# Performance work log

Measured on AMD Instinct MI355X. Metric: run time of the kernel, lower is better.

The kernel has to match this reference:

```python
import jax, jax.numpy as jnp
import numpy as np

B = 4096   # batch_size from init_kwargs
D = 128    # embedding dim
TEMP = 0.25


def _l2_normalize(x, eps=1e-12):
    # matches F.normalize(dim=1): x / max(||x||, eps)
    n = jnp.linalg.norm(x, axis=1, keepdims=True)
    return x / jnp.maximum(n, eps)


def setup_inputs() -> dict:
    key = jax.random.key(0)
    k1, k2 = jax.random.split(key)
    return {
        "emb_i": jax.random.normal(k1, (B, D), dtype=jnp.float32),
        "emb_j": jax.random.normal(k2, (B, D), dtype=jnp.float32),
    }


def reference(emb_i, emb_j):
    b = emb_i.shape[0]
    z_i = _l2_normalize(emb_i)
    z_j = _l2_normalize(emb_j)
    reps = jnp.concatenate([z_i, z_j], axis=0)            # [2B, D]
    # cosine similarity of normalized vectors == dot product
    sim = reps @ reps.T                                    # [2B, 2B]
    sim_ij = jnp.diagonal(sim, offset=b)                   # [B]
    sim_ji = jnp.diagonal(sim, offset=-b)                  # [B]
    positives = jnp.concatenate([sim_ij, sim_ji], axis=0)  # [2B]
    # negatives_mask as overwritten in __init__: ones only on the two
    # off-diagonal cross-view blocks.
    mask = (
        jnp.zeros((2 * b, 2 * b), dtype=sim.dtype)
        .at[:b, b:].set(1.0)
        .at[b:, :b].set(1.0)
    )
    exp_sim = jnp.exp(sim / TEMP)                          # [2B, 2B]
    denom = jnp.sum(mask * exp_sim, axis=1)                # [2B]
    loss_partial = -jnp.log(jnp.exp(positives / TEMP) / denom)
    loss = jnp.sum(loss_partial) / (2 * b)
    return loss
```

## Files before the change

kernel.cpp:

```cpp
#include <hip/hip_runtime.h>
#include <hip/hip_bf16.h>

#define BATCH 4096
#define DIM   128
#define EXP_SCALE 5.770780163555854f

typedef __bf16 bf16_t;
typedef __bf16 bf16x8 __attribute__((ext_vector_type(8)));
typedef float  f32x4  __attribute__((ext_vector_type(4)));

__global__ __launch_bounds__(256) void normalize_kernel(
    const float* __restrict__ emb_i, const float* __restrict__ emb_j,
    bf16_t* __restrict__ zi, bf16_t* __restrict__ zj, float* __restrict__ pos)
{
    int wave = threadIdx.x >> 6;
    int lane = threadIdx.x & 63;
    int k = blockIdx.x * 4 + wave;

    const float2* ei = (const float2*)(emb_i + (size_t)k * DIM);
    const float2* ej = (const float2*)(emb_j + (size_t)k * DIM);
    float2 a = ei[lane];
    float2 b = ej[lane];

    float sii = a.x * a.x + a.y * a.y;
    float sjj = b.x * b.x + b.y * b.y;
    float sij = a.x * b.x + a.y * b.y;
#pragma unroll
    for (int m = 1; m < 64; m <<= 1) {
        sii += __shfl_xor(sii, m);
        sjj += __shfl_xor(sjj, m);
        sij += __shfl_xor(sij, m);
    }
    float inv_i = 1.0f / fmaxf(sqrtf(sii), 1e-12f);
    float inv_j = 1.0f / fmaxf(sqrtf(sjj), 1e-12f);

    struct bf16_2 { bf16_t x, y; };
    bf16_2 pi, pj;
    pi.x = (bf16_t)(a.x * inv_i);  pi.y = (bf16_t)(a.y * inv_i);
    pj.x = (bf16_t)(b.x * inv_j);  pj.y = (bf16_t)(b.y * inv_j);
    ((bf16_2*)(zi + (size_t)k * DIM))[lane] = pi;
    ((bf16_2*)(zj + (size_t)k * DIM))[lane] = pj;

    if (lane == 0) pos[k] = sij * inv_i * inv_j;
}

__global__ __launch_bounds__(256) void gemm_exp_kernel(
    const bf16_t* __restrict__ zi, const bf16_t* __restrict__ zj,
    float* __restrict__ rowDenom, float* __restrict__ colDenom)
{
    __shared__ __align__(16) bf16_t zi_s[128][136];
    __shared__ __align__(16) bf16_t zj_s[128][136];

    const int tid = threadIdx.x;
    const int ti = blockIdx.x, tj = blockIdx.y;

#pragma unroll
    for (int it = 0; it < 8; ++it) {
        int c = it * 256 + tid;
        int row = c >> 4;
        int col = (c & 15) << 3;
        *(uint4*)&zi_s[row][col] =
            *(const uint4*)(zi + ((size_t)(ti * 128 + row)) * DIM + col);
        *(uint4*)&zj_s[row][col] =
            *(const uint4*)(zj + ((size_t)(tj * 128 + row)) * DIM + col);
    }
    __syncthreads();

    const int wave = tid >> 6;
    const int lane = tid & 63;
    const int l15  = lane & 15;
    const int quad = lane >> 4;

    const f32x4 vzero = {0.f, 0.f, 0.f, 0.f};
    f32x4 acc[2][8];
#pragma unroll
    for (int rt = 0; rt < 2; ++rt)
#pragma unroll
        for (int ct = 0; ct < 8; ++ct) acc[rt][ct] = vzero;

#pragma unroll
    for (int ks = 0; ks < 4; ++ks) {
        int k0 = ks * 32 + quad * 8;
        bf16x8 afrag[2], bfrag[8];
#pragma unroll
        for (int rt = 0; rt < 2; ++rt)
            afrag[rt] = *(const bf16x8*)&zi_s[(wave * 2 + rt) * 16 + l15][k0];
#pragma unroll
        for (int ct = 0; ct < 8; ++ct)
            bfrag[ct] = *(const bf16x8*)&zj_s[ct * 16 + l15][k0];
#pragma unroll
        for (int rt = 0; rt < 2; ++rt)
#pragma unroll
            for (int ct = 0; ct < 8; ++ct)
                acc[rt][ct] = __builtin_amdgcn_mfma_f32_16x16x32_bf16(
                    afrag[rt], bfrag[ct], acc[rt][ct], 0, 0, 0);
    }

    float rowPart[2][4] = {{0.f, 0.f, 0.f, 0.f}, {0.f, 0.f, 0.f, 0.f}};
    float colPart[8]    = {0.f, 0.f, 0.f, 0.f, 0.f, 0.f, 0.f, 0.f};
#pragma unroll
    for (int rt = 0; rt < 2; ++rt)
#pragma unroll
        for (int ct = 0; ct < 8; ++ct)
#pragma unroll
            for (int r = 0; r < 4; ++r) {
                float e = exp2f(acc[rt][ct][r] * EXP_SCALE);
                rowPart[rt][r] += e;
                colPart[ct]    += e;
            }

#pragma unroll
    for (int rt = 0; rt < 2; ++rt)
#pragma unroll
        for (int r = 0; r < 4; ++r) {
            float v = rowPart[rt][r];
            v += __shfl_xor(v, 1);
            v += __shfl_xor(v, 2);
            v += __shfl_xor(v, 4);
            v += __shfl_xor(v, 8);
            if (l15 == 0) {
                int grow = ti * 128 + (wave * 2 + rt) * 16 + quad * 4 + r;
                atomicAdd(&rowDenom[grow], v);
            }
        }

#pragma unroll
    for (int ct = 0; ct < 8; ++ct) {
        float v = colPart[ct];
        v += __shfl_xor(v, 16);
        v += __shfl_xor(v, 32);
        if (quad == 0) {
            int gcol = tj * 128 + ct * 16 + l15;
            atomicAdd(&colDenom[gcol], v);
        }
    }
}

__global__ __launch_bounds__(256) void finalize_kernel(
    const float* __restrict__ rowDenom, const float* __restrict__ colDenom,
    const float* __restrict__ pos, float* __restrict__ out)
{
    int tid = threadIdx.x;
    float acc = 0.f;
    for (int k = tid; k < BATCH; k += 256)
        acc += logf(rowDenom[k]) + logf(colDenom[k]) - 8.0f * pos[k];
#pragma unroll
    for (int m = 1; m < 64; m <<= 1) acc += __shfl_xor(acc, m);
    __shared__ float red[4];
    if ((tid & 63) == 0) red[tid >> 6] = acc;
    __syncthreads();
    if (tid == 0)
        out[0] = (red[0] + red[1] + red[2] + red[3]) * (1.0f / (2.0f * BATCH));
}

extern "C" void kernel_launch(void* const* d_in, const int* in_sizes, int n_in,
                              void* d_out, int out_size, void* d_ws, size_t ws_size,
                              hipStream_t stream) {
    const float* emb_i = (const float*)d_in[0];
    const float* emb_j = (const float*)d_in[1];
    float* out = (float*)d_out;

    char* ws = (char*)d_ws;
    bf16_t* zi       = (bf16_t*)(ws);
    bf16_t* zj       = (bf16_t*)(ws + (1u << 20));
    float*  rowDenom = (float*)(ws + (2u << 20));
    float*  colDenom = rowDenom + BATCH;
    float*  pos      = colDenom + BATCH;

    hipMemsetAsync(rowDenom, 0, 2 * BATCH * sizeof(float), stream);
    normalize_kernel<<<BATCH / 4, 256, 0, stream>>>(emb_i, emb_j, zi, zj, pos);
    gemm_exp_kernel<<<dim3(32, 32), 256, 0, stream>>>(zi, zj, rowDenom, colDenom);
    finalize_kernel<<<1, 256, 0, stream>>>(rowDenom, colDenom, pos, out);
}
```

Before: 83.22 us.

## Fuse normalization into GEMM tile load and replace atomics with partial-sum buffers

Each GEMM block now loads fp32 embeddings directly, L2-normalizes rows in registers and writes bf16 into shared memory, which removes the separate normalize kernel and the memset. Positives are taken from the diagonal of the diagonal tiles rather than computed separately. Row and column denominators are written as per-tile partials without atomics, and a 1024-thread finalize reduces them. The cost is that every block redundantly normalizes its 128-row tiles, 32 times per row, and reads twice as many bytes per tile in fp32. Positives now use bf16-rounded values instead of fp32 dot products, and the finalize must read 1 MB of partials.

```diff
diff --git a/kernel.cpp b/kernel.cpp
--- a/kernel.cpp
+++ b/kernel.cpp
@@ -3,66 +3,52 @@
 
 #define BATCH 4096
 #define DIM   128
+#define NT    32
 #define EXP_SCALE 5.770780163555854f
 
 typedef __bf16 bf16_t;
 typedef __bf16 bf16x8 __attribute__((ext_vector_type(8)));
 typedef float  f32x4  __attribute__((ext_vector_type(4)));
 
-__global__ __launch_bounds__(256) void normalize_kernel(
+__global__ __launch_bounds__(256) void fused_kernel(
     const float* __restrict__ emb_i, const float* __restrict__ emb_j,
-    bf16_t* __restrict__ zi, bf16_t* __restrict__ zj, float* __restrict__ pos)
-{
-    int wave = threadIdx.x >> 6;
-    int lane = threadIdx.x & 63;
-    int k = blockIdx.x * 4 + wave;
-
-    const float2* ei = (const float2*)(emb_i + (size_t)k * DIM);
-    const float2* ej = (const float2*)(emb_j + (size_t)k * DIM);
-    float2 a = ei[lane];
-    float2 b = ej[lane];
-
-    float sii = a.x * a.x + a.y * a.y;
-    float sjj = b.x * b.x + b.y * b.y;
-    float sij = a.x * b.x + a.y * b.y;
-#pragma unroll
-    for (int m = 1; m < 64; m <<= 1) {
-        sii += __shfl_xor(sii, m);
-        sjj += __shfl_xor(sjj, m);
-        sij += __shfl_xor(sij, m);
-    }
-    float inv_i = 1.0f / fmaxf(sqrtf(sii), 1e-12f);
-    float inv_j = 1.0f / fmaxf(sqrtf(sjj), 1e-12f);
-
-    struct bf16_2 { bf16_t x, y; };
-    bf16_2 pi, pj;
-    pi.x = (bf16_t)(a.x * inv_i);  pi.y = (bf16_t)(a.y * inv_i);
-    pj.x = (bf16_t)(b.x * inv_j);  pj.y = (bf16_t)(b.y * inv_j);
-    ((bf16_2*)(zi + (size_t)k * DIM))[lane] = pi;
-    ((bf16_2*)(zj + (size_t)k * DIM))[lane] = pj;
-
-    if (lane == 0) pos[k] = sij * inv_i * inv_j;
-}
-
-__global__ __launch_bounds__(256) void gemm_exp_kernel(
-    const bf16_t* __restrict__ zi, const bf16_t* __restrict__ zj,
-    float* __restrict__ rowDenom, float* __restrict__ colDenom)
+    float* __restrict__ pr, float* __restrict__ pc, float* __restrict__ pos)
 {
     __shared__ __align__(16) bf16_t zi_s[128][136];
     __shared__ __align__(16) bf16_t zj_s[128][136];
+    __shared__ float colRed[4][128];
 
     const int tid = threadIdx.x;
     const int ti = blockIdx.x, tj = blockIdx.y;
 
+    const int g  = tid >> 4;
+    const int gl = tid & 15;
+
 #pragma unroll
-    for (int it = 0; it < 8; ++it) {
-        int c = it * 256 + tid;
-        int row = c >> 4;
-        int col = (c & 15) << 3;
-        *(uint4*)&zi_s[row][col] =
-            *(const uint4*)(zi + ((size_t)(ti * 128 + row)) * DIM + col);
-        *(uint4*)&zj_s[row][col] =
-            *(const uint4*)(zj + ((size_t)(tj * 128 + row)) * DIM + col);
+    for (int m = 0; m < 2; ++m) {
+        const float* src = m ? emb_j : emb_i;
+        const int rbase = (m ? tj : ti) * 128;
+        bf16_t (*dst)[136] = m ? zj_s : zi_s;
+#pragma unroll
+        for (int it = 0; it < 8; ++it) {
+            int row = it * 16 + g;
+            const float4* p = (const float4*)(src + (size_t)(rbase + row) * DIM);
+            float4 a = p[gl * 2];
+            float4 b = p[gl * 2 + 1];
+            float ss = a.x*a.x + a.y*a.y + a.z*a.z + a.w*a.w
+                     + b.x*b.x + b.y*b.y + b.z*b.z + b.w*b.w;
+            ss += __shfl_xor(ss, 1);
+            ss += __shfl_xor(ss, 2);
+            ss += __shfl_xor(ss, 4);
+            ss += __shfl_xor(ss, 8);
+            float inv = 1.0f / fmaxf(sqrtf(ss), 1e-12f);
+            bf16x8 o;
+            o[0] = (bf16_t)(a.x * inv); o[1] = (bf16_t)(a.y * inv);
+            o[2] = (bf16_t)(a.z * inv); o[3] = (bf16_t)(a.w * inv);
+            o[4] = (bf16_t)(b.x * inv); o[5] = (bf16_t)(b.y * inv);
+            o[6] = (bf16_t)(b.z * inv); o[7] = (bf16_t)(b.w * inv);
+            *(bf16x8*)&dst[row][gl * 8] = o;
+        }
     }
     __syncthreads();
 
@@ -96,6 +82,19 @@
                     afrag[rt], bfrag[ct], acc[rt][ct], 0, 0, 0);
     }
 
+    if (ti == tj) {
+#pragma unroll
+        for (int rt = 0; rt < 2; ++rt)
+#pragma unroll
+            for (int ct = 0; ct < 8; ++ct)
+#pragma unroll
+                for (int r = 0; r < 4; ++r) {
+                    int rr = (wave * 2 + rt) * 16 + quad * 4 + r;
+                    int cc = ct * 16 + l15;
+                    if (rr == cc) pos[ti * 128 + rr] = acc[rt][ct][r];
+                }
+    }
+
     float rowPart[2][4] = {{0.f, 0.f, 0.f, 0.f}, {0.f, 0.f, 0.f, 0.f}};
     float colPart[8]    = {0.f, 0.f, 0.f, 0.f, 0.f, 0.f, 0.f, 0.f};
 #pragma unroll
@@ -120,7 +119,7 @@
             v += __shfl_xor(v, 8);
             if (l15 == 0) {
                 int grow = ti * 128 + (wave * 2 + rt) * 16 + quad * 4 + r;
-                atomicAdd(&rowDenom[grow], v);
+                pr[tj * BATCH + grow] = v;
             }
         }
 
@@ -129,28 +128,43 @@
         float v = colPart[ct];
         v += __shfl_xor(v, 16);
         v += __shfl_xor(v, 32);
-        if (quad == 0) {
-            int gcol = tj * 128 + ct * 16 + l15;
-            atomicAdd(&colDenom[gcol], v);
-        }
+        if (quad == 0) colRed[wave][ct * 16 + l15] = v;
+    }
+    __syncthreads();
+    if (tid < 128) {
+        float s = colRed[0][tid] + colRed[1][tid] + colRed[2][tid] + colRed[3][tid];
+        pc[ti * BATCH + tj * 128 + tid] = s;
     }
 }
 
-__global__ __launch_bounds__(256) void finalize_kernel(
-    const float* __restrict__ rowDenom, const float* __restrict__ colDenom,
+__global__ __launch_bounds__(1024) void finalize_kernel(
+    const float* __restrict__ pr, const float* __restrict__ pc,
     const float* __restrict__ pos, float* __restrict__ out)
 {
     int tid = threadIdx.x;
     float acc = 0.f;
-    for (int k = tid; k < BATCH; k += 256)
-        acc += logf(rowDenom[k]) + logf(colDenom[k]) - 8.0f * pos[k];
+#pragma unroll
+    for (int it = 0; it < 4; ++it) {
+        int k = it * 1024 + tid;
+        float sR = 0.f, sC = 0.f;
+#pragma unroll
+        for (int t = 0; t < NT; ++t) {
+            sR += pr[t * BATCH + k];
+            sC += pc[t * BATCH + k];
+        }
+        acc += logf(sR) + logf(sC) - 8.0f * pos[k];
+    }
 #pragma unroll
     for (int m = 1; m < 64; m <<= 1) acc += __shfl_xor(acc, m);
-    __shared__ float red[4];
+    __shared__ float red[16];
     if ((tid & 63) == 0) red[tid >> 6] = acc;
     __syncthreads();
-    if (tid == 0)
-        out[0] = (red[0] + red[1] + red[2] + red[3]) * (1.0f / (2.0f * BATCH));
+    if (tid == 0) {
+        float s = 0.f;
+#pragma unroll
+        for (int w = 0; w < 16; ++w) s += red[w];
+        out[0] = s * (1.0f / (2.0f * BATCH));
+    }
 }
 
 extern "C" void kernel_launch(void* const* d_in, const int* in_sizes, int n_in,
@@ -161,14 +175,10 @@
     float* out = (float*)d_out;
 
     char* ws = (char*)d_ws;
-    bf16_t* zi       = (bf16_t*)(ws);
-    bf16_t* zj       = (bf16_t*)(ws + (1u << 20));
-    float*  rowDenom = (float*)(ws + (2u << 20));
-    float*  colDenom = rowDenom + BATCH;
-    float*  pos      = colDenom + BATCH;
+    float* pr  = (float*)(ws);
+    float* pc  = (float*)(ws + (size_t)NT * BATCH * 4);
+    float* pos = (float*)(ws + (size_t)2 * NT * BATCH * 4);
 
-    hipMemsetAsync(rowDenom, 0, 2 * BATCH * sizeof(float), stream);
-    normalize_kernel<<<BATCH / 4, 256, 0, stream>>>(emb_i, emb_j, zi, zj, pos);
-    gemm_exp_kernel<<<dim3(32, 32), 256, 0, stream>>>(zi, zj, rowDenom, colDenom);
-    finalize_kernel<<<1, 256, 0, stream>>>(rowDenom, colDenom, pos, out);
+    fused_kernel<<<dim3(NT, NT), 256, 0, stream>>>(emb_i, emb_j, pr, pc, pos);
+    finalize_kernel<<<1, 1024, 0, stream>>>(pr, pc, pos, out);
 }
```

Result: slower. 88.40 us (+6.2%).

## Fold denominator zeroing into normalize kernel and pre-reduce column sums in LDS

Applied to the files above, without the earlier changes.

The separate memset launch goes away, and the denominator buffer is now zeroed by the first 16 blocks of the normalize kernel. In the GEMM kernel, the per-wave column partial sums are combined through shared memory, so each block issues 128 column atomics instead of 512. The finalize loop is fully unrolled. These changes cut one launch and reduce atomic traffic, at the cost of an extra block-wide sync in the GEMM epilogue.

```diff
diff --git a/kernel.cpp b/kernel.cpp
--- a/kernel.cpp
+++ b/kernel.cpp
@@ -3,6 +3,7 @@
 
 #define BATCH 4096
 #define DIM   128
+#define NT    32
 #define EXP_SCALE 5.770780163555854f
 
 typedef __bf16 bf16_t;
@@ -11,8 +12,14 @@
 
 __global__ __launch_bounds__(256) void normalize_kernel(
     const float* __restrict__ emb_i, const float* __restrict__ emb_j,
-    bf16_t* __restrict__ zi, bf16_t* __restrict__ zj, float* __restrict__ pos)
+    bf16_t* __restrict__ zi, bf16_t* __restrict__ zj, float* __restrict__ pos,
+    float* __restrict__ denoms )
 {
+    if (blockIdx.x < 16) {
+        int idx = (blockIdx.x * 256 + threadIdx.x) * 4;
+        *(float4*)&denoms[idx] = make_float4(0.f, 0.f, 0.f, 0.f);
+    }
+
     int wave = threadIdx.x >> 6;
     int lane = threadIdx.x & 63;
     int k = blockIdx.x * 4 + wave;
@@ -50,6 +57,7 @@
 {
     __shared__ __align__(16) bf16_t zi_s[128][136];
     __shared__ __align__(16) bf16_t zj_s[128][136];
+    __shared__ float colRed[4][128];
 
     const int tid = threadIdx.x;
     const int ti = blockIdx.x, tj = blockIdx.y;
@@ -129,21 +137,28 @@
         float v = colPart[ct];
         v += __shfl_xor(v, 16);
         v += __shfl_xor(v, 32);
-        if (quad == 0) {
-            int gcol = tj * 128 + ct * 16 + l15;
-            atomicAdd(&colDenom[gcol], v);
-        }
+        if (quad == 0) colRed[wave][ct * 16 + l15] = v;
+    }
+    __syncthreads();
+    if (tid < 128) {
+        float s = colRed[0][tid] + colRed[1][tid] + colRed[2][tid] + colRed[3][tid];
+        atomicAdd(&colDenom[tj * 128 + tid], s);
     }
 }
 
 __global__ __launch_bounds__(256) void finalize_kernel(
-    const float* __restrict__ rowDenom, const float* __restrict__ colDenom,
-    const float* __restrict__ pos, float* __restrict__ out)
+    const float* __restrict__ denoms, const float* __restrict__ pos,
+    float* __restrict__ out)
 {
+    const float* rowDenom = denoms;
+    const float* colDenom = denoms + BATCH;
     int tid = threadIdx.x;
     float acc = 0.f;
-    for (int k = tid; k < BATCH; k += 256)
+#pragma unroll
+    for (int it = 0; it < 16; ++it) {
+        int k = it * 256 + tid;
         acc += logf(rowDenom[k]) + logf(colDenom[k]) - 8.0f * pos[k];
+    }
 #pragma unroll
     for (int m = 1; m < 64; m <<= 1) acc += __shfl_xor(acc, m);
     __shared__ float red[4];
@@ -161,14 +176,12 @@
     float* out = (float*)d_out;
 
     char* ws = (char*)d_ws;
-    bf16_t* zi       = (bf16_t*)(ws);
-    bf16_t* zj       = (bf16_t*)(ws + (1u << 20));
-    float*  rowDenom = (float*)(ws + (2u << 20));
-    float*  colDenom = rowDenom + BATCH;
-    float*  pos      = colDenom + BATCH;
+    bf16_t* zi     = (bf16_t*)(ws);
+    bf16_t* zj     = (bf16_t*)(ws + (1u << 20));
+    float*  denoms = (float*)(ws + (2u << 20));
+    float*  pos    = denoms + 2 * BATCH;
 
-    hipMemsetAsync(rowDenom, 0, 2 * BATCH * sizeof(float), stream);
-    normalize_kernel<<<BATCH / 4, 256, 0, stream>>>(emb_i, emb_j, zi, zj, pos);
-    gemm_exp_kernel<<<dim3(32, 32), 256, 0, stream>>>(zi, zj, rowDenom, colDenom);
-    finalize_kernel<<<1, 256, 0, stream>>>(rowDenom, colDenom, pos, out);
+    normalize_kernel<<<BATCH / 4, 256, 0, stream>>>(emb_i, emb_j, zi, zj, pos, denoms);
+    gemm_exp_kernel<<<dim3(NT, NT), 256, 0, stream>>>(zi, zj, denoms, denoms + BATCH);
+    finalize_kernel<<<1, 256, 0, stream>>>(denoms, pos, out);
 }
```

New measurement: 74.60 us. 1.12x faster.
